# Kernel tuning notes

Measured on AMD Instinct MI355X. Metric: run time of the kernel, lower is better.

The kernel has to match this reference:

```python
import jax, jax.numpy as jnp
import numpy as np

CH = 512
CK = CH // 8  # 64

def conv1x1(w, x):
    # w: [out, in], x: [B, in, H, W] -> [B, out, H, W]
    return jnp.einsum('oc,bchw->bohw', w, x)

def maxpool2(x):
    B, C, H, W = x.shape
    return x.reshape(B, C, H // 2, 2, W // 2, 2).max(axis=(3, 5))

def setup_inputs() -> dict:
    key = jax.random.key(0)
    ks = jax.random.split(key, 5)
    B, H, W = 16, 64, 64
    x = jax.random.normal(ks[0], (B, CH, H, W), dtype=jnp.float32)
    scale = 1.0 / np.sqrt(CH)
    Wt = jax.random.normal(ks[1], (CK, CH), dtype=jnp.float32) * scale
    Wp = jax.random.normal(ks[2], (CK, CH), dtype=jnp.float32) * scale
    Wg = jax.random.normal(ks[3], (CK, CH), dtype=jnp.float32) * scale
    Wo = jax.random.normal(ks[4], (CH, CK), dtype=jnp.float32) * (1.0 / np.sqrt(CK))
    gamma = jnp.float32(0.1)  # nonzero so backward through attention path is exercised
    return {'x': x, 'Wt': Wt, 'Wp': Wp, 'Wg': Wg, 'Wo': Wo, 'gamma': gamma}

def reference(x, Wt, Wp, Wg, Wo, gamma):
    B, C, H, W = x.shape
    N = H * W          # query positions
    M = N // 4         # pooled key/value positions
    theta = conv1x1(Wt, x).reshape(B, CK, N)            # [B, ck, N]
    phi = maxpool2(conv1x1(Wp, x)).reshape(B, CK, M)    # [B, ck, M]
    g = maxpool2(conv1x1(Wg, x)).reshape(B, CK, M)      # [B, ck, M]
    scores = jnp.einsum('bcn,bcm->bnm', theta, phi)     # [B, N, M]
    beta = jax.nn.softmax(scores, axis=-1)
    o = jnp.einsum('bcm,bnm->bcn', g, beta)             # [B, ck, N]
    o = conv1x1(Wo, o.reshape(B, CK, H, W))             # [B, C, H, W]
    return gamma * o + x
```

## Files before the change

kernel.cpp:

```cpp
#include <hip/hip_runtime.h>

#define CHN 512
#define CKD 64
#define NPOS 4096
#define MPOS 1024

typedef __attribute__((ext_vector_type(8))) short bf16x8;
typedef __attribute__((ext_vector_type(4))) float f32x4;
typedef __attribute__((ext_vector_type(8))) unsigned short u16x8;

static constexpr size_t OFF_O   = 0;
static constexpr size_t OFF_THT = 4194304;
static constexpr size_t OFF_PHT = 6291456;
static constexpr size_t OFF_GB  = 6815744;
static constexpr size_t OFF_WBF = 7340032;
static constexpr size_t OFF_WOB = 7389184;

__device__ __forceinline__ unsigned short f2bf(float f) {
  union { float f; unsigned int u; } v; v.f = f;
  unsigned int r = v.u + 0x7FFFu + ((v.u >> 16) & 1u);
  return (unsigned short)(r >> 16);
}

__device__ __forceinline__ void gl2lds16(const void* g, void* l) {
  __builtin_amdgcn_global_load_lds(
      (const __attribute__((address_space(1))) unsigned int*)g,
      (__attribute__((address_space(3))) unsigned int*)l, 16, 0, 0);
}

__global__ __launch_bounds__(256) void prep_w_kernel(
    const float* __restrict__ Wt, const float* __restrict__ Wp,
    const float* __restrict__ Wg, const float* __restrict__ Wo,
    unsigned short* __restrict__ wbf, unsigned short* __restrict__ wobf)
{
  int id = blockIdx.x * 256 + threadIdx.x;
  if (id < 98304) {
    int mat = id >> 15, r = id & 32767;
    const float* W = (mat == 0) ? Wt : (mat == 1) ? Wp : Wg;
    wbf[id] = f2bf(W[r]);
  } else {
    int j = id - 98304;
    wobf[j] = f2bf(Wo[j]);
  }
}

__global__ __launch_bounds__(256) void qkv_fused_kernel(
    const float* __restrict__ x,
    const unsigned short* __restrict__ wbf,
    unsigned short* __restrict__ thT, unsigned short* __restrict__ phT,
    unsigned short* __restrict__ gbf)
{
  __shared__ unsigned short sXb[64 * 132];
  __shared__ unsigned short sW[3 * 64 * 64];

  const int bx = blockIdx.x;
  const int b  = blockIdx.y;
  const int t  = threadIdx.x;
  const int w   = t >> 6;
  const int l   = t & 63;
  const int l16 = l & 15;
  const int lhi = l >> 4;
  const int n0  = bx * 128;

  const float* xb = x + (size_t)b * CHN * NPOS + n0;

  f32x4 acc[3][2][4];
#pragma unroll
  for (int m = 0; m < 3; ++m)
#pragma unroll
    for (int nf = 0; nf < 2; ++nf)
#pragma unroll
      for (int ckf = 0; ckf < 4; ++ckf) acc[m][nf][ckf] = (f32x4){0.f, 0.f, 0.f, 0.f};

  for (int c0 = 0; c0 < CHN; c0 += 64) {
    if (c0) __syncthreads();
#pragma unroll
    for (int i = 0; i < 8; ++i) {
      int row  = i * 8 + (t >> 5);
      int col4 = t & 31;
      float4 v = *(const float4*)(xb + (size_t)(c0 + row) * NPOS + col4 * 4);
      ushort4 u;
      u.x = f2bf(v.x); u.y = f2bf(v.y); u.z = f2bf(v.z); u.w = f2bf(v.w);
      *(ushort4*)&sXb[row * 132 + col4 * 4] = u;
    }
#pragma unroll
    for (int mi = 0; mi < 6; ++mi) {
      int mat = mi >> 1;
      int row = ((mi & 1) * 4 + w) * 8 + (l >> 3);
      int sbyte = (l & 7) * 16;
      const char* g = (const char*)wbf +
          ((((size_t)mat * 64 + row) * CHN + c0) << 1) + (sbyte ^ ((row & 7) << 4));
      gl2lds16(g, (char*)sW + mi * 4096 + w * 1024);
    }
    __syncthreads();

#pragma unroll
    for (int ks = 0; ks < 2; ++ks) {
      const int cu = ks * 32 + lhi * 8;
      bf16x8 a[2];
#pragma unroll
      for (int nf = 0; nf < 2; ++nf) {
        const int rn = 16 * w + 64 * nf + l16;
        bf16x8 av;
#pragma unroll
        for (int e = 0; e < 8; ++e)
          av[e] = (short)sXb[(cu + e) * 132 + rn];
        a[nf] = av;
      }
#pragma unroll
      for (int m = 0; m < 3; ++m)
#pragma unroll
        for (int ckf = 0; ckf < 4; ++ckf) {
          int rw = ckf * 16 + l16;
          bf16x8 bb = *(const bf16x8*)&sW[m * 4096 + rw * 64 + ((ks * 32 + lhi * 8) ^ ((rw & 7) * 8))];
          acc[m][0][ckf] = __builtin_amdgcn_mfma_f32_16x16x32_bf16(a[0], bb, acc[m][0][ckf], 0, 0, 0);
          acc[m][1][ckf] = __builtin_amdgcn_mfma_f32_16x16x32_bf16(a[1], bb, acc[m][1][ckf], 0, 0, 0);
        }
    }
  }

  unsigned short* th = thT + (size_t)b * NPOS * 64;
#pragma unroll
  for (int nf = 0; nf < 2; ++nf)
#pragma unroll
    for (int r = 0; r < 4; ++r) {
      int n = n0 + 16 * w + 64 * nf + lhi * 4 + r;
#pragma unroll
      for (int ckf = 0; ckf < 4; ++ckf)
        th[(size_t)n * 64 + ckf * 16 + l16] = f2bf(acc[0][nf][ckf][r]);
    }

  unsigned short* ph = phT + (size_t)b * MPOS * 64;
  unsigned short* gb = gbf + (size_t)b * CKD * MPOS;
#pragma unroll
  for (int pr = 0; pr < 2; ++pr) {
    int mcol = bx * 32 + 8 * w + lhi * 2 + pr;
#pragma unroll
    for (int ckf = 0; ckf < 4; ++ckf) {
      int ck = ckf * 16 + l16;
      float vp = fmaxf(fmaxf(acc[1][0][ckf][2 * pr], acc[1][0][ckf][2 * pr + 1]),
                       fmaxf(acc[1][1][ckf][2 * pr], acc[1][1][ckf][2 * pr + 1]));
      float vg = fmaxf(fmaxf(acc[2][0][ckf][2 * pr], acc[2][0][ckf][2 * pr + 1]),
                       fmaxf(acc[2][1][ckf][2 * pr], acc[2][1][ckf][2 * pr + 1]));
      ph[(size_t)mcol * 64 + ck] = f2bf(vp);
      gb[(size_t)ck * MPOS + mcol] = f2bf(vg);
    }
  }
}

__global__ __launch_bounds__(256) void attn_kernel(
    const unsigned short* __restrict__ thT,
    const unsigned short* __restrict__ phT,
    const unsigned short* __restrict__ gbf,
    unsigned short* __restrict__ obf)
{
  __shared__ unsigned short sTh[128 * 64];
  __shared__ unsigned short sP [128 * 64];
  __shared__ unsigned short sPhi[64 * 64];
  __shared__ unsigned short sG [64 * 64];

  const int qt = blockIdx.x;
  const int b  = blockIdx.y;
  const int t  = threadIdx.x;
  const int w   = t >> 6;
  const int l   = t & 63;
  const int l16 = l & 15;
  const int lhi = l >> 4;

  {
    const char* srcb = (const char*)(thT + ((size_t)b * NPOS + (size_t)qt * 128) * 64);
#pragma unroll
    for (int i = 0; i < 4; ++i) {
      int cidx = i * 256 + t;
      int row = cidx >> 3, sub = cidx & 7;
      gl2lds16(srcb + row * 128 + ((sub * 16) ^ ((row & 7) << 4)),
               (char*)sTh + (i * 256 + w * 64) * 16);
    }
  }

  f32x4 oacc[2][4];
  float m_run[2][4], l_run[2][4];
#pragma unroll
  for (int qf = 0; qf < 2; ++qf)
#pragma unroll
    for (int i = 0; i < 4; ++i) {
      oacc[qf][i] = (f32x4){0.f, 0.f, 0.f, 0.f};
      m_run[qf][i] = -1e30f; l_run[qf][i] = 0.f;
    }

  const unsigned short* phb = phT + (size_t)b * MPOS * 64;
  const unsigned short* gb  = gbf + (size_t)b * CKD * MPOS;

  for (int mt = 0; mt < 16; ++mt) {
    __syncthreads();
#pragma unroll
    for (int i = 0; i < 2; ++i) {
      int cidx = i * 256 + t;
      int row = cidx >> 3, sub = cidx & 7;
      gl2lds16((const char*)(phb + (size_t)(mt * 64 + row) * 64) +
                   ((sub * 16) ^ ((row & 7) << 4)),
               (char*)sPhi + (i * 256 + w * 64) * 16);
      gl2lds16((const char*)(gb + (size_t)row * MPOS + mt * 64) +
                   ((sub * 16) ^ ((row & 7) << 4)),
               (char*)sG + (i * 256 + w * 64) * 16);
    }
    __syncthreads();

    f32x4 sacc[2][4];
#pragma unroll
    for (int qf = 0; qf < 2; ++qf)
#pragma unroll
      for (int mf = 0; mf < 4; ++mf) sacc[qf][mf] = (f32x4){0.f, 0.f, 0.f, 0.f};
#pragma unroll
    for (int qf = 0; qf < 2; ++qf)
#pragma unroll
      for (int ks = 0; ks < 2; ++ks) {
        const int q  = 32 * w + 16 * qf + l16;
        const int ob = lhi * 8 + 32 * ks;
        bf16x8 a = *(const bf16x8*)&sTh[q * 64 + (ob ^ ((q & 7) * 8))];
#pragma unroll
        for (int mf = 0; mf < 4; ++mf) {
          const int m = l16 + 16 * mf;
          bf16x8 bb = *(const bf16x8*)&sPhi[m * 64 + (ob ^ ((m & 7) * 8))];
          sacc[qf][mf] = __builtin_amdgcn_mfma_f32_16x16x32_bf16(a, bb, sacc[qf][mf], 0, 0, 0);
        }
      }

    float sc[2][4];
#pragma unroll
    for (int qf = 0; qf < 2; ++qf) {
#pragma unroll
      for (int r = 0; r < 4; ++r) {
        float mx = fmaxf(fmaxf(sacc[qf][0][r], sacc[qf][1][r]),
                         fmaxf(sacc[qf][2][r], sacc[qf][3][r]));
        mx = fmaxf(mx, __shfl_xor(mx, 1, 16));
        mx = fmaxf(mx, __shfl_xor(mx, 2, 16));
        mx = fmaxf(mx, __shfl_xor(mx, 4, 16));
        mx = fmaxf(mx, __shfl_xor(mx, 8, 16));
        float mnew = fmaxf(m_run[qf][r], mx);
        sc[qf][r] = __expf(m_run[qf][r] - mnew);
        m_run[qf][r] = mnew;
        float rs = 0.f;
#pragma unroll
        for (int mf = 0; mf < 4; ++mf) {
          float p = __expf(sacc[qf][mf][r] - mnew);
          sacc[qf][mf][r] = p;
          rs += p;
        }
        rs += __shfl_xor(rs, 1, 16);
        rs += __shfl_xor(rs, 2, 16);
        rs += __shfl_xor(rs, 4, 16);
        rs += __shfl_xor(rs, 8, 16);
        l_run[qf][r] = l_run[qf][r] * sc[qf][r] + rs;
      }
#pragma unroll
      for (int r = 0; r < 4; ++r) {
        const int qq = 32 * w + 16 * qf + lhi * 4 + r;
        const int swz = (qq & 7) * 8;
#pragma unroll
        for (int mf = 0; mf < 4; ++mf) {
          const int m = l16 + 16 * mf;
          sP[qq * 64 + ((m & 0x38) ^ swz) + (m & 7)] = f2bf(sacc[qf][mf][r]);
        }
      }
    }

#pragma unroll
    for (int qf = 0; qf < 2; ++qf)
#pragma unroll
      for (int ckf = 0; ckf < 4; ++ckf)
#pragma unroll
        for (int r = 0; r < 4; ++r) oacc[qf][ckf][r] *= sc[qf][r];

#pragma unroll
    for (int qf = 0; qf < 2; ++qf)
#pragma unroll
      for (int ks = 0; ks < 2; ++ks) {
        const int q  = 32 * w + 16 * qf + l16;
        const int ob = lhi * 8 + 32 * ks;
        bf16x8 a = *(const bf16x8*)&sP[q * 64 + (ob ^ ((q & 7) * 8))];
#pragma unroll
        for (int ckf = 0; ckf < 4; ++ckf) {
          const int ck = l16 + 16 * ckf;
          bf16x8 bb = *(const bf16x8*)&sG[ck * 64 + (ob ^ ((ck & 7) * 8))];
          oacc[qf][ckf] = __builtin_amdgcn_mfma_f32_16x16x32_bf16(a, bb, oacc[qf][ckf], 0, 0, 0);
        }
      }
  }

  unsigned short* ob = obf + (size_t)b * NPOS * 64;
#pragma unroll
  for (int qf = 0; qf < 2; ++qf) {
    float inv[4];
#pragma unroll
    for (int r = 0; r < 4; ++r) inv[r] = 1.0f / l_run[qf][r];
#pragma unroll
    for (int r = 0; r < 4; ++r) {
      int n = qt * 128 + 32 * w + 16 * qf + lhi * 4 + r;
#pragma unroll
      for (int ckf = 0; ckf < 4; ++ckf)
        ob[(size_t)n * 64 + ckf * 16 + l16] = f2bf(oacc[qf][ckf][r] * inv[r]);
    }
  }
}

__global__ __launch_bounds__(256) void outconv_mfma_kernel(
    const float* __restrict__ x,
    const unsigned short* __restrict__ wobf,
    const unsigned short* __restrict__ obf,
    const float* __restrict__ gamma_p, float* __restrict__ outp)
{
  __shared__ unsigned short sO[256 * 64];
  __shared__ unsigned short sWo[64 * 64];

  const int nt = blockIdx.x;
  const int ct = blockIdx.y;
  const int b  = blockIdx.z;
  const int t  = threadIdx.x;
  const int w   = t >> 6;
  const int l   = t & 63;
  const int l16 = l & 15;
  const int lhi = l >> 4;

#pragma unroll
  for (int i = 0; i < 8; ++i) {
    int cidx = i * 256 + t;
    int row = cidx >> 3, sub = cidx & 7;
    const char* g = (const char*)obf +
        ((((size_t)b * NPOS + nt * 256 + row) * 64) << 1) + ((sub * 16) ^ ((row & 7) << 4));
    gl2lds16(g, (char*)sO + (i * 256 + w * 64) * 16);
  }
#pragma unroll
  for (int i = 0; i < 2; ++i) {
    int cidx = i * 256 + t;
    int row = cidx >> 3, sub = cidx & 7;
    const char* g = (const char*)wobf +
        ((((size_t)(ct * 64 + row)) * 64) << 1) + ((sub * 16) ^ ((row & 7) << 4));
    gl2lds16(g, (char*)sWo + (i * 256 + w * 64) * 16);
  }

  const float gv = *gamma_p;
  float4 xv[4][4];
#pragma unroll
  for (int nf = 0; nf < 4; ++nf) {
    const int n = nt * 256 + w * 64 + nf * 16 + lhi * 4;
#pragma unroll
    for (int cf = 0; cf < 4; ++cf) {
      const int co = ct * 64 + cf * 16 + l16;
      xv[nf][cf] = *(const float4*)(x + ((size_t)b * CHN + co) * NPOS + n);
    }
  }
  __syncthreads();

  f32x4 acc[4][4];
#pragma unroll
  for (int nf = 0; nf < 4; ++nf)
#pragma unroll
    for (int cf = 0; cf < 4; ++cf) acc[nf][cf] = (f32x4){0.f, 0.f, 0.f, 0.f};

#pragma unroll
  for (int ks = 0; ks < 2; ++ks) {
    const int cu = ks * 32 + lhi * 8;
    bf16x8 a[4];
#pragma unroll
    for (int nf = 0; nf < 4; ++nf) {
      int rn = w * 64 + nf * 16 + l16;
      a[nf] = *(const bf16x8*)&sO[rn * 64 + (cu ^ ((rn & 7) * 8))];
    }
#pragma unroll
    for (int cf = 0; cf < 4; ++cf) {
      int rw = cf * 16 + l16;
      bf16x8 bb = *(const bf16x8*)&sWo[rw * 64 + (cu ^ ((rw & 7) * 8))];
#pragma unroll
      for (int nf = 0; nf < 4; ++nf)
        acc[nf][cf] = __builtin_amdgcn_mfma_f32_16x16x32_bf16(a[nf], bb, acc[nf][cf], 0, 0, 0);
    }
  }

#pragma unroll
  for (int nf = 0; nf < 4; ++nf) {
    const int n = nt * 256 + w * 64 + nf * 16 + lhi * 4;
#pragma unroll
    for (int cf = 0; cf < 4; ++cf) {
      const int co = ct * 64 + cf * 16 + l16;
      const size_t off = ((size_t)b * CHN + co) * NPOS + n;
      float4 rr;
      rr.x = fmaf(gv, acc[nf][cf][0], xv[nf][cf].x);
      rr.y = fmaf(gv, acc[nf][cf][1], xv[nf][cf].y);
      rr.z = fmaf(gv, acc[nf][cf][2], xv[nf][cf].z);
      rr.w = fmaf(gv, acc[nf][cf][3], xv[nf][cf].w);
      *(float4*)(outp + off) = rr;
    }
  }
}

extern "C" void kernel_launch(void* const* d_in, const int* in_sizes, int n_in,
                              void* d_out, int out_size, void* d_ws, size_t ws_size,
                              hipStream_t stream)
{
  const float* x     = (const float*)d_in[0];
  const float* Wt    = (const float*)d_in[1];
  const float* Wp    = (const float*)d_in[2];
  const float* Wg    = (const float*)d_in[3];
  const float* Wo    = (const float*)d_in[4];
  const float* gamma = (const float*)d_in[5];
  float* out = (float*)d_out;
  float* ws  = (float*)d_ws;

  unsigned short* obf = (unsigned short*)(ws + OFF_O);
  unsigned short* thT = (unsigned short*)(ws + OFF_THT);
  unsigned short* phT = (unsigned short*)(ws + OFF_PHT);
  unsigned short* gbf = (unsigned short*)(ws + OFF_GB);
  unsigned short* wbf = (unsigned short*)(ws + OFF_WBF);
  unsigned short* wob = (unsigned short*)(ws + OFF_WOB);

  prep_w_kernel<<<dim3(512), 256, 0, stream>>>(Wt, Wp, Wg, Wo, wbf, wob);
  qkv_fused_kernel<<<dim3(32, 16), 256, 0, stream>>>(x, wbf, thT, phT, gbf);
  attn_kernel<<<dim3(32, 16), 256, 0, stream>>>(thT, phT, gbf, obf);
  outconv_mfma_kernel<<<dim3(16, 8, 16), 256, 0, stream>>>(x, wob, obf, gamma, out);
}
```

Measured before the change: 142.1 us.

## Fuse output 1x1 conv and residual into attention kernel epilogue

Merges the attention kernel and the output-projection kernel into one. The normalized attention output is written to shared memory (reusing the P buffer) instead of global memory. Wo tiles are streamed into the reused theta buffer, and the projection, gamma scaling and residual add are done in place. This removes the bf16 intermediate write and read plus one launch, but leaves the epilogue's large x/out traffic on 512 blocks instead of 2048.

```diff
diff --git a/kernel.cpp b/kernel.cpp
--- a/kernel.cpp
+++ b/kernel.cpp
@@ -9,7 +9,6 @@
 typedef __attribute__((ext_vector_type(4))) float f32x4;
 typedef __attribute__((ext_vector_type(8))) unsigned short u16x8;
 
-static constexpr size_t OFF_O   = 0;
 static constexpr size_t OFF_THT = 4194304;
 static constexpr size_t OFF_PHT = 6291456;
 static constexpr size_t OFF_GB  = 6815744;
@@ -148,11 +147,14 @@
   }
 }
 
-__global__ __launch_bounds__(256) void attn_kernel(
+__global__ __launch_bounds__(256) void attn_out_kernel(
     const unsigned short* __restrict__ thT,
     const unsigned short* __restrict__ phT,
     const unsigned short* __restrict__ gbf,
-    unsigned short* __restrict__ obf)
+    const unsigned short* __restrict__ wobf,
+    const float* __restrict__ x,
+    const float* __restrict__ gamma_p,
+    float* __restrict__ outp)
 {
   __shared__ unsigned short sTh[128 * 64];
   __shared__ unsigned short sP [128 * 64];
@@ -288,7 +290,6 @@
       }
   }
 
-  unsigned short* ob = obf + (size_t)b * NPOS * 64;
 #pragma unroll
   for (int qf = 0; qf < 2; ++qf) {
     float inv[4];
@@ -296,100 +297,70 @@
     for (int r = 0; r < 4; ++r) inv[r] = 1.0f / l_run[qf][r];
 #pragma unroll
     for (int r = 0; r < 4; ++r) {
-      int n = qt * 128 + 32 * w + 16 * qf + lhi * 4 + r;
-#pragma unroll
-      for (int ckf = 0; ckf < 4; ++ckf)
-        ob[(size_t)n * 64 + ckf * 16 + l16] = f2bf(oacc[qf][ckf][r] * inv[r]);
-    }
-  }
-}
-
-__global__ __launch_bounds__(256) void outconv_mfma_kernel(
-    const float* __restrict__ x,
-    const unsigned short* __restrict__ wobf,
-    const unsigned short* __restrict__ obf,
-    const float* __restrict__ gamma_p, float* __restrict__ outp)
-{
-  __shared__ unsigned short sO[256 * 64];
-  __shared__ unsigned short sWo[64 * 64];
-
-  const int nt = blockIdx.x;
-  const int ct = blockIdx.y;
-  const int b  = blockIdx.z;
-  const int t  = threadIdx.x;
-  const int w   = t >> 6;
-  const int l   = t & 63;
-  const int l16 = l & 15;
-  const int lhi = l >> 4;
-
-#pragma unroll
-  for (int i = 0; i < 8; ++i) {
-    int cidx = i * 256 + t;
-    int row = cidx >> 3, sub = cidx & 7;
-    const char* g = (const char*)obf +
-        ((((size_t)b * NPOS + nt * 256 + row) * 64) << 1) + ((sub * 16) ^ ((row & 7) << 4));
-    gl2lds16(g, (char*)sO + (i * 256 + w * 64) * 16);
-  }
-#pragma unroll
-  for (int i = 0; i < 2; ++i) {
-    int cidx = i * 256 + t;
-    int row = cidx >> 3, sub = cidx & 7;
-    const char* g = (const char*)wobf +
-        ((((size_t)(ct * 64 + row)) * 64) << 1) + ((sub * 16) ^ ((row & 7) << 4));
-    gl2lds16(g, (char*)sWo + (i * 256 + w * 64) * 16);
-  }
-
+      const int qq = 32 * w + 16 * qf + lhi * 4 + r;
+      const int swz = (qq & 7) * 8;
+#pragma unroll
+      for (int ckf = 0; ckf < 4; ++ckf) {
+        const int ck = l16 + 16 * ckf;
+        sP[qq * 64 + ((ck & 0x38) ^ swz) + (ck & 7)] = f2bf(oacc[qf][ckf][r] * inv[r]);
+      }
+    }
+  }
+
+  unsigned short* sWoL = sTh;
   const float gv = *gamma_p;
-  float4 xv[4][4];
-#pragma unroll
-  for (int nf = 0; nf < 4; ++nf) {
-    const int n = nt * 256 + w * 64 + nf * 16 + lhi * 4;
-#pragma unroll
-    for (int cf = 0; cf < 4; ++cf) {
-      const int co = ct * 64 + cf * 16 + l16;
-      xv[nf][cf] = *(const float4*)(x + ((size_t)b * CHN + co) * NPOS + n);
-    }
-  }
-  __syncthreads();
-
-  f32x4 acc[4][4];
-#pragma unroll
-  for (int nf = 0; nf < 4; ++nf)
-#pragma unroll
-    for (int cf = 0; cf < 4; ++cf) acc[nf][cf] = (f32x4){0.f, 0.f, 0.f, 0.f};
-
-#pragma unroll
-  for (int ks = 0; ks < 2; ++ks) {
-    const int cu = ks * 32 + lhi * 8;
-    bf16x8 a[4];
-#pragma unroll
-    for (int nf = 0; nf < 4; ++nf) {
-      int rn = w * 64 + nf * 16 + l16;
-      a[nf] = *(const bf16x8*)&sO[rn * 64 + (cu ^ ((rn & 7) * 8))];
-    }
-#pragma unroll
-    for (int cf = 0; cf < 4; ++cf) {
-      int rw = cf * 16 + l16;
-      bf16x8 bb = *(const bf16x8*)&sWo[rw * 64 + (cu ^ ((rw & 7) * 8))];
-#pragma unroll
-      for (int nf = 0; nf < 4; ++nf)
-        acc[nf][cf] = __builtin_amdgcn_mfma_f32_16x16x32_bf16(a[nf], bb, acc[nf][cf], 0, 0, 0);
-    }
-  }
-
-#pragma unroll
-  for (int nf = 0; nf < 4; ++nf) {
-    const int n = nt * 256 + w * 64 + nf * 16 + lhi * 4;
-#pragma unroll
-    for (int cf = 0; cf < 4; ++cf) {
-      const int co = ct * 64 + cf * 16 + l16;
-      const size_t off = ((size_t)b * CHN + co) * NPOS + n;
-      float4 rr;
-      rr.x = fmaf(gv, acc[nf][cf][0], xv[nf][cf].x);
-      rr.y = fmaf(gv, acc[nf][cf][1], xv[nf][cf].y);
-      rr.z = fmaf(gv, acc[nf][cf][2], xv[nf][cf].z);
-      rr.w = fmaf(gv, acc[nf][cf][3], xv[nf][cf].w);
-      *(float4*)(outp + off) = rr;
+
+  for (int cc = 0; cc < 4; ++cc) {
+    __syncthreads();
+#pragma unroll
+    for (int i = 0; i < 4; ++i) {
+      int cidx = i * 256 + t;
+      int row = cidx >> 3, sub = cidx & 7;
+      gl2lds16((const char*)wobf + (((size_t)(cc * 128 + row)) * 64 << 1) +
+                   ((sub * 16) ^ ((row & 7) << 4)),
+               (char*)sWoL + (i * 256 + w * 64) * 16);
+    }
+    __syncthreads();
+
+    f32x4 acc[2][8];
+#pragma unroll
+    for (int qf = 0; qf < 2; ++qf)
+#pragma unroll
+      for (int cf = 0; cf < 8; ++cf) acc[qf][cf] = (f32x4){0.f, 0.f, 0.f, 0.f};
+
+#pragma unroll
+    for (int ks = 0; ks < 2; ++ks) {
+      const int cu = ks * 32 + lhi * 8;
+      bf16x8 a[2];
+#pragma unroll
+      for (int qf = 0; qf < 2; ++qf) {
+        const int q = 32 * w + 16 * qf + l16;
+        a[qf] = *(const bf16x8*)&sP[q * 64 + (cu ^ ((q & 7) * 8))];
+      }
+#pragma unroll
+      for (int cf = 0; cf < 8; ++cf) {
+        const int rw = cf * 16 + l16;
+        bf16x8 bb = *(const bf16x8*)&sWoL[rw * 64 + (cu ^ ((rw & 7) * 8))];
+        acc[0][cf] = __builtin_amdgcn_mfma_f32_16x16x32_bf16(a[0], bb, acc[0][cf], 0, 0, 0);
+        acc[1][cf] = __builtin_amdgcn_mfma_f32_16x16x32_bf16(a[1], bb, acc[1][cf], 0, 0, 0);
+      }
+    }
+
+#pragma unroll
+    for (int qf = 0; qf < 2; ++qf) {
+      const int n = qt * 128 + 32 * w + 16 * qf + lhi * 4;
+#pragma unroll
+      for (int cf = 0; cf < 8; ++cf) {
+        const int co = cc * 128 + cf * 16 + l16;
+        const size_t off = ((size_t)b * CHN + co) * NPOS + n;
+        float4 xv = *(const float4*)(x + off);
+        float4 rr;
+        rr.x = fmaf(gv, acc[qf][cf][0], xv.x);
+        rr.y = fmaf(gv, acc[qf][cf][1], xv.y);
+        rr.z = fmaf(gv, acc[qf][cf][2], xv.z);
+        rr.w = fmaf(gv, acc[qf][cf][3], xv.w);
+        *(float4*)(outp + off) = rr;
+      }
     }
   }
 }
@@ -407,7 +378,6 @@
   float* out = (float*)d_out;
   float* ws  = (float*)d_ws;
 
-  unsigned short* obf = (unsigned short*)(ws + OFF_O);
   unsigned short* thT = (unsigned short*)(ws + OFF_THT);
   unsigned short* phT = (unsigned short*)(ws + OFF_PHT);
   unsigned short* gbf = (unsigned short*)(ws + OFF_GB);
@@ -416,6 +386,5 @@
 
   prep_w_kernel<<<dim3(512), 256, 0, stream>>>(Wt, Wp, Wg, Wo, wbf, wob);
   qkv_fused_kernel<<<dim3(32, 16), 256, 0, stream>>>(x, wbf, thT, phT, gbf);
-  attn_kernel<<<dim3(32, 16), 256, 0, stream>>>(thT, phT, gbf, obf);
-  outconv_mfma_kernel<<<dim3(16, 8, 16), 256, 0, stream>>>(x, wob, obf, gamma, out);
-}
+  attn_out_kernel<<<dim3(32, 16), 256, 0, stream>>>(thT, phT, gbf, wob, x, gamma, out);
+}
```

Result: slower. 155.4 us (+9.4%).

## Prefetch next x and phi/g tiles into registers during compute

Applied to the files above, without the earlier changes.

In the projection kernel, the next 64-channel slab of x is loaded into registers while the current slab's MFMAs run, then converted to bf16 and written to LDS at the start of the following iteration. In the attention kernel, the phi and g tile loads move from direct global-to-LDS copies to register-staged loads issued one iteration ahead, then stored to swizzled LDS. The aim is to hide global memory latency behind the matrix work. The cost is extra VGPRs for the staging buffers, which may lower occupancy, and the attention path gives up the async direct-to-LDS path.

```diff
diff --git a/kernel.cpp b/kernel.cpp
--- a/kernel.cpp
+++ b/kernel.cpp
@@ -63,6 +63,8 @@
   const int n0  = bx * 128;
 
   const float* xb = x + (size_t)b * CHN * NPOS + n0;
+  const int xrow = t >> 5;
+  const int xcol4 = t & 31;
 
   f32x4 acc[3][2][4];
 #pragma unroll
@@ -71,18 +73,14 @@
     for (int nf = 0; nf < 2; ++nf)
 #pragma unroll
       for (int ckf = 0; ckf < 4; ++ckf) acc[m][nf][ckf] = (f32x4){0.f, 0.f, 0.f, 0.f};
+
+  float4 xR[8];
+#pragma unroll
+  for (int i = 0; i < 8; ++i)
+    xR[i] = *(const float4*)(xb + (size_t)(i * 8 + xrow) * NPOS + xcol4 * 4);
 
   for (int c0 = 0; c0 < CHN; c0 += 64) {
     if (c0) __syncthreads();
-#pragma unroll
-    for (int i = 0; i < 8; ++i) {
-      int row  = i * 8 + (t >> 5);
-      int col4 = t & 31;
-      float4 v = *(const float4*)(xb + (size_t)(c0 + row) * NPOS + col4 * 4);
-      ushort4 u;
-      u.x = f2bf(v.x); u.y = f2bf(v.y); u.z = f2bf(v.z); u.w = f2bf(v.w);
-      *(ushort4*)&sXb[row * 132 + col4 * 4] = u;
-    }
 #pragma unroll
     for (int mi = 0; mi < 6; ++mi) {
       int mat = mi >> 1;
@@ -92,7 +90,20 @@
           ((((size_t)mat * 64 + row) * CHN + c0) << 1) + (sbyte ^ ((row & 7) << 4));
       gl2lds16(g, (char*)sW + mi * 4096 + w * 1024);
     }
+#pragma unroll
+    for (int i = 0; i < 8; ++i) {
+      ushort4 u;
+      u.x = f2bf(xR[i].x); u.y = f2bf(xR[i].y);
+      u.z = f2bf(xR[i].z); u.w = f2bf(xR[i].w);
+      *(ushort4*)&sXb[(i * 8 + xrow) * 132 + xcol4 * 4] = u;
+    }
     __syncthreads();
+
+    if (c0 + 64 < CHN) {
+#pragma unroll
+      for (int i = 0; i < 8; ++i)
+        xR[i] = *(const float4*)(xb + (size_t)(c0 + 64 + i * 8 + xrow) * NPOS + xcol4 * 4);
+    }
 
 #pragma unroll
     for (int ks = 0; ks < 2; ++ks) {
@@ -112,7 +123,7 @@
 #pragma unroll
         for (int ckf = 0; ckf < 4; ++ckf) {
           int rw = ckf * 16 + l16;
-          bf16x8 bb = *(const bf16x8*)&sW[m * 4096 + rw * 64 + ((ks * 32 + lhi * 8) ^ ((rw & 7) * 8))];
+          bf16x8 bb = *(const bf16x8*)&sW[m * 4096 + rw * 64 + (cu ^ ((rw & 7) * 8))];
           acc[m][0][ckf] = __builtin_amdgcn_mfma_f32_16x16x32_bf16(a[0], bb, acc[m][0][ckf], 0, 0, 0);
           acc[m][1][ckf] = __builtin_amdgcn_mfma_f32_16x16x32_bf16(a[1], bb, acc[m][1][ckf], 0, 0, 0);
         }
@@ -191,20 +202,35 @@
   const unsigned short* phb = phT + (size_t)b * MPOS * 64;
   const unsigned short* gb  = gbf + (size_t)b * CKD * MPOS;
 
+  const int srow = t >> 3;
+  const int ssub = t & 7;
+  u16x8 phR[2], gR[2];
+#pragma unroll
+  for (int i = 0; i < 2; ++i) {
+    int row = i * 32 + srow;
+    phR[i] = *(const u16x8*)(phb + (size_t)row * 64 + ssub * 8);
+    gR[i]  = *(const u16x8*)(gb + (size_t)row * MPOS + ssub * 8);
+  }
+
   for (int mt = 0; mt < 16; ++mt) {
     __syncthreads();
 #pragma unroll
     for (int i = 0; i < 2; ++i) {
-      int cidx = i * 256 + t;
-      int row = cidx >> 3, sub = cidx & 7;
-      gl2lds16((const char*)(phb + (size_t)(mt * 64 + row) * 64) +
-                   ((sub * 16) ^ ((row & 7) << 4)),
-               (char*)sPhi + (i * 256 + w * 64) * 16);
-      gl2lds16((const char*)(gb + (size_t)row * MPOS + mt * 64) +
-                   ((sub * 16) ^ ((row & 7) << 4)),
-               (char*)sG + (i * 256 + w * 64) * 16);
+      int row = i * 32 + srow;
+      int off = row * 64 + ((ssub * 8) ^ ((row & 7) * 8));
+      *(u16x8*)&sPhi[off] = phR[i];
+      *(u16x8*)&sG[off]   = gR[i];
     }
     __syncthreads();
+
+    if (mt + 1 < 16) {
+#pragma unroll
+      for (int i = 0; i < 2; ++i) {
+        int row = i * 32 + srow;
+        phR[i] = *(const u16x8*)(phb + (size_t)((mt + 1) * 64 + row) * 64 + ssub * 8);
+        gR[i]  = *(const u16x8*)(gb + (size_t)row * MPOS + (mt + 1) * 64 + ssub * 8);
+      }
+    }
 
     f32x4 sacc[2][4];
 #pragma unroll
```

Result: no change. 141.1 us (-0.8%).
